# Kernel tuning notes

Measured on AMD Instinct MI355X. Metric: run time of the kernel, lower is better.

Reference implementation:

```python
import jax, jax.numpy as jnp
import numpy as np


def conv2d(x, w, b=None, stride=1, padding=0, groups=1, dilation=1):
    out = jax.lax.conv_general_dilated(
        x, w, (stride, stride), [(padding, padding), (padding, padding)],
        rhs_dilation=(dilation, dilation),
        dimension_numbers=("NCHW", "OIHW", "NCHW"),
        feature_group_count=groups)
    if b is not None:
        out = out + b[None, :, None, None]
    return out


def _l2norm(x, axis=-1, eps=1e-12):
    n = jnp.sqrt(jnp.sum(x * x, axis=axis, keepdims=True))
    return x / jnp.maximum(n, eps)


def setup_inputs() -> dict:
    B, C, H, W = 8, 384, 64, 64
    heads = 8
    C6, C2, C4 = C // 6, C // 2, C // 4
    key = jax.random.key(0)
    ks = iter(jax.random.split(key, 40))
    p = lambda shape: jax.random.normal(next(ks), shape, jnp.float32) * 0.02
    z = lambda n: jnp.zeros((n,), jnp.float32)
    inp = {
        "x": jax.random.normal(next(ks), (B, C, H, W), jnp.float32),
        "temperature": jnp.ones((heads, 1, 1), jnp.float32),
        "qkv_w": p((3 * C, C)),
        "proj_w": p((C, C)), "proj_b": z(C),
        # dwconv branch on v_: 1x1 conv then depthwise 3x3
        "dw1_w": p((C, C, 1, 1)), "dw1_b": z(C),
        "dw2_w": p((C, 1, 3, 3)), "dw2_b": z(C),
        # ChannelProjection
        "cp_in_w": p((C6, C, 1, 1)), "cp_in_b": z(C6),
        "ci1_w": p((C6, C6, 1, 1)), "ci1_b": z(C6),
        "ci2a_w": p((C6, 1, 3, 3)), "ci2a_b": z(C6),
        "ci2b_w": p((C6, 1, 7, 7)), "ci2b_b": z(C6),
        "ci2c_w": p((C6, C6, 1, 1)), "ci2c_b": z(C6),
        "cp_out_w": p((C, C6, 1, 1)), "cp_out_b": z(C),
        # SpatialProjection
        "sp_in_w": p((C2, C, 1, 1)), "sp_in_b": z(C2),
        "sp_dw_w": p((C2, 1, 3, 3)), "sp_dw_b": z(C2),
        "sp_out_w": p((C, C4, 1, 1)), "sp_out_b": z(C),
    }
    return inp


def reference(x, temperature, qkv_w, proj_w, proj_b, dw1_w, dw1_b, dw2_w, dw2_b,
              cp_in_w, cp_in_b, ci1_w, ci1_b, ci2a_w, ci2a_b, ci2b_w, ci2b_b,
              ci2c_w, ci2c_b, cp_out_w, cp_out_b, sp_in_w, sp_in_b,
              sp_dw_w, sp_dw_b, sp_out_w, sp_out_b):
    B, C, H, W = x.shape
    N = H * W
    heads = temperature.shape[0]
    hd = C // heads
    C6 = cp_in_w.shape[0]
    C2 = sp_in_w.shape[0]

    xf = x.reshape(B, C, N).transpose(0, 2, 1)            # (B,N,C)
    qkv = xf @ qkv_w.T                                     # (B,N,3C)
    qkv = qkv.reshape(B, N, 3, heads, hd).transpose(2, 0, 3, 1, 4)  # (3,B,h,N,hd)
    q = qkv[0].swapaxes(-2, -1)                            # (B,h,hd,N)
    k = qkv[1].swapaxes(-2, -1)
    v = qkv[2].swapaxes(-2, -1)
    v_ = v.reshape(B, C, H, W)

    q = _l2norm(q, axis=-1)
    k = _l2norm(k, axis=-1)
    attn = jnp.einsum("bhcn,bhdn->bhcd", q, k) * temperature  # (B,h,hd,hd)
    attn = jax.nn.softmax(attn, axis=-1)
    at = jnp.einsum("bhcd,bhdn->bhcn", attn, v)             # (B,h,hd,N)
    attened = at.transpose(0, 3, 1, 2).reshape(B, N, C)     # (B,N,C)

    conv_x = conv2d(conv2d(v_, dw1_w, dw1_b),
                    dw2_w, dw2_b, padding=1, groups=C)      # (B,C,H,W)

    # ChannelProjection on attention map
    ar = attened.swapaxes(-2, -1).reshape(B, C, H, W)
    t = conv2d(ar, cp_in_w, cp_in_b)                        # (B,C6,H,W)
    ci1 = conv2d(t.mean((2, 3), keepdims=True), ci1_w, ci1_b)  # (B,C6,1,1)
    ci2 = conv2d(t, ci2a_w, ci2a_b, padding=1, groups=C6)
    ci2 = conv2d(ci2, ci2b_w, ci2b_b, padding=9, groups=C6, dilation=3)
    ci2 = conv2d(ci2, ci2c_w, ci2c_b)
    channel_map = conv2d(t * ci1 * ci2, cp_out_w, cp_out_b)  # (B,C,H,W)

    attened = attened + channel_map.transpose(0, 2, 3, 1).reshape(B, N, C)
    cm = channel_map.mean((2, 3), keepdims=True)            # (B,C,1,1)

    # SpatialProjection on conv branch
    sp = conv2d(conv_x, sp_in_w, sp_in_b)                   # (B,C2,H,W)
    d = conv2d(sp, sp_dw_w, sp_dw_b, padding=1, groups=C2)
    x1, x2 = jnp.split(d, 2, axis=1)
    sp = conv2d(jax.nn.gelu(x1, approximate=False) * x2, sp_out_w, sp_out_b)
    spatial_map = sp.transpose(0, 2, 3, 1).reshape(B, N, C)

    attened = attened * jax.nn.sigmoid(spatial_map)
    conv_x = conv_x * jax.nn.sigmoid(cm)
    conv_x = conv_x.transpose(0, 2, 3, 1).reshape(B, N, C)

    out = (attened + conv_x) @ proj_w.T + proj_b            # (B,N,C)
    return out.transpose(0, 2, 1).reshape(B, C, H, W)
```

## Files before the change

### kernel.cpp

```cpp
#include <hip/hip_runtime.h>
#include <hip/hip_bf16.h>

typedef __bf16 bf16;
typedef __bf16 bf16x8 __attribute__((ext_vector_type(8)));
typedef float f32x4 __attribute__((ext_vector_type(4)));

#define N4 4096
#define CCH 384

struct CvtArgs {
    const float* src[9];
    bf16* dst[9];
    long gpre[10];
};

__global__ __launch_bounds__(256) void cvt_kernel(CvtArgs a, long totalGroups)
{
    long g = (long)blockIdx.x * 256 + threadIdx.x;
    if (g >= totalGroups) return;
    int lo = 0, hi = 8;
    while (lo < hi) { int mid = (lo + hi) >> 1; if (g >= a.gpre[mid + 1]) lo = mid + 1; else hi = mid; }
    long off = (g - a.gpre[lo]) << 3;
    const float* s = a.src[lo] + off;
    float4 v0 = *(const float4*)s;
    float4 v1 = *(const float4*)(s + 4);
    bf16x8 o;
    o[0] = (bf16)v0.x; o[1] = (bf16)v0.y; o[2] = (bf16)v0.z; o[3] = (bf16)v0.w;
    o[4] = (bf16)v1.x; o[5] = (bf16)v1.y; o[6] = (bf16)v1.z; o[7] = (bf16)v1.w;
    *(bf16x8*)(a.dst[lo] + off) = o;
}

__global__ __launch_bounds__(256) void gemm_bf16_kernel(
    const bf16* __restrict__ Wg, const bf16* __restrict__ Xg,
    const float* __restrict__ bias, void* __restrict__ Og,
    int K, long xStride, long oStride, int f32out)
{
    constexpr int LDP = 40;
    __shared__ bf16 Wt[64 * LDP];
    __shared__ bf16 Xt[64 * LDP];
    const int t = threadIdx.x;
    const int lin = blockIdx.x;
    const int b = lin & 7;
    const int rest = lin >> 3;
    const int nBase = (rest & 63) << 6;
    const int mBase = (rest >> 6) << 6;
    const bf16* Xb = Xg + (long)b * xStride;
    const int lane = t & 63, wv = t >> 6;
    const int wm = (wv >> 1) << 5, wn = (wv & 1) << 5;
    const int lr = lane & 15, qd = lane >> 4;
    const int wlm = t >> 2, wlk = (t & 3) << 3;
    const int xln = t & 63, xlk = (t >> 6) << 3;

    f32x4 acc[2][2] = {};

    for (int k0 = 0; k0 < K; k0 += 32) {
        bf16x8 wvv = *(const bf16x8*)(Wg + (long)(mBase + wlm) * K + k0 + wlk);
        const bf16* xp = Xb + (long)(k0 + xlk) * N4 + nBase + xln;
        bf16x8 xvv;
        #pragma unroll
        for (int j = 0; j < 8; j++) xvv[j] = xp[(long)j * N4];

        __syncthreads();
        *(bf16x8*)(&Wt[wlm * LDP + wlk]) = wvv;
        *(bf16x8*)(&Xt[xln * LDP + xlk]) = xvv;
        __syncthreads();

        bf16x8 af[2], bfr[2];
        #pragma unroll
        for (int i = 0; i < 2; i++) {
            af[i]  = *(const bf16x8*)(&Wt[(wm + i * 16 + lr) * LDP + qd * 8]);
            bfr[i] = *(const bf16x8*)(&Xt[(wn + i * 16 + lr) * LDP + qd * 8]);
        }
        #pragma unroll
        for (int i = 0; i < 2; i++)
            #pragma unroll
            for (int j = 0; j < 2; j++)
                acc[i][j] = __builtin_amdgcn_mfma_f32_16x16x32_bf16(
                    af[i], bfr[j], acc[i][j], 0, 0, 0);
    }

    #pragma unroll
    for (int i = 0; i < 2; i++)
        #pragma unroll
        for (int j = 0; j < 2; j++)
            #pragma unroll
            for (int r = 0; r < 4; r++) {
                int row = mBase + wm + i * 16 + qd * 4 + r;
                int col = nBase + wn + j * 16 + lr;
                float v = acc[i][j][r];
                if (bias) v += bias[row];
                long oi = (long)b * oStride + (long)row * N4 + col;
                if (f32out) ((float*)Og)[oi] = v;
                else        ((bf16*)Og)[oi] = (bf16)v;
            }
}

__global__ __launch_bounds__(256) void gemm128_kernel(
    const bf16* __restrict__ Wg, const bf16* __restrict__ Xg,
    const float* __restrict__ bias, void* __restrict__ Og,
    int K, long xStride, long oStride, int f32out)
{
    constexpr int LDP = 40;
    __shared__ bf16 Wt[128 * LDP];
    __shared__ bf16 Xt[128 * LDP];
    const int t = threadIdx.x;
    const int lin = blockIdx.x;
    const int b = lin & 7;
    const int rest = lin >> 3;
    const int nBase = (rest & 31) << 7;
    const int mBase = (rest >> 5) << 7;
    const bf16* Xb = Xg + (long)b * xStride;
    const int lane = t & 63, wv = t >> 6;
    const int wm = (wv >> 1) << 6, wn = (wv & 1) << 6;
    const int lr = lane & 15, qd = lane >> 4;
    const int wrow0 = t >> 2, wk = (t & 3) << 3;

    f32x4 acc[4][4] = {};

    for (int k0 = 0; k0 < K; k0 += 32) {
        bf16x8 wv0 = *(const bf16x8*)(Wg + (long)(mBase + wrow0) * K + k0 + wk);
        bf16x8 wv1 = *(const bf16x8*)(Wg + (long)(mBase + wrow0 + 64) * K + k0 + wk);
        bf16x8 xv[2];
        #pragma unroll
        for (int g = 0; g < 2; g++) {
            int slot = g * 256 + t;
            int kg = slot >> 7, nn = slot & 127;
            const bf16* xp = Xb + (long)(k0 + kg * 8) * N4 + nBase + nn;
            #pragma unroll
            for (int j = 0; j < 8; j++) xv[g][j] = xp[(long)j * N4];
        }
        __syncthreads();
        *(bf16x8*)(&Wt[wrow0 * LDP + wk]) = wv0;
        *(bf16x8*)(&Wt[(wrow0 + 64) * LDP + wk]) = wv1;
        #pragma unroll
        for (int g = 0; g < 2; g++) {
            int slot = g * 256 + t;
            int kg = slot >> 7, nn = slot & 127;
            *(bf16x8*)(&Xt[nn * LDP + kg * 8]) = xv[g];
        }
        __syncthreads();

        bf16x8 af[4], bfr[4];
        #pragma unroll
        for (int i = 0; i < 4; i++) {
            af[i]  = *(const bf16x8*)(&Wt[(wm + i * 16 + lr) * LDP + qd * 8]);
            bfr[i] = *(const bf16x8*)(&Xt[(wn + i * 16 + lr) * LDP + qd * 8]);
        }
        #pragma unroll
        for (int i = 0; i < 4; i++)
            #pragma unroll
            for (int j = 0; j < 4; j++)
                acc[i][j] = __builtin_amdgcn_mfma_f32_16x16x32_bf16(
                    af[i], bfr[j], acc[i][j], 0, 0, 0);
    }

    #pragma unroll
    for (int i = 0; i < 4; i++)
        #pragma unroll
        for (int j = 0; j < 4; j++)
            #pragma unroll
            for (int r = 0; r < 4; r++) {
                int row = mBase + wm + i * 16 + qd * 4 + r;
                int col = nBase + wn + j * 16 + lr;
                float v = acc[i][j][r];
                if (bias) v += bias[row];
                long oi = (long)b * oStride + (long)row * N4 + col;
                if (f32out) ((float*)Og)[oi] = v;
                else        ((bf16*)Og)[oi] = (bf16)v;
            }
}

__global__ __launch_bounds__(256) void rownorm_kernel(
    const bf16* __restrict__ qkv, float* __restrict__ invn)
{
    const int c = blockIdx.x, b = blockIdx.y;
    const bf16* p = qkv + (long)b * 3 * CCH * N4 + (long)c * N4;
    float s = 0.f;
    for (int i = threadIdx.x * 8; i < N4; i += 2048) {
        bf16x8 v = *(const bf16x8*)(p + i);
        #pragma unroll
        for (int e = 0; e < 8; e++) { float f = (float)v[e]; s += f * f; }
    }
    #pragma unroll
    for (int o = 32; o; o >>= 1) s += __shfl_down(s, o, 64);
    __shared__ float red[4];
    if ((threadIdx.x & 63) == 0) red[threadIdx.x >> 6] = s;
    __syncthreads();
    if (threadIdx.x == 0) {
        float tot = red[0] + red[1] + red[2] + red[3];
        invn[b * 768 + c] = 1.0f / fmaxf(sqrtf(tot), 1e-12f);
    }
}

__global__ __launch_bounds__(256) void attn_logits_kernel(
    const bf16* __restrict__ qkv, float* __restrict__ part)
{
    const int kc = blockIdx.x;
    const int bh = blockIdx.y;
    const int b = bh >> 3, h = bh & 7;
    const int t = threadIdx.x, lane = t & 63, wv = t >> 6;
    const int lr = lane & 15, qd = lane >> 4;
    const bf16* qb = qkv + (long)b * 3 * CCH * N4 + (long)h * 48 * N4;
    const bf16* kb = qb + (long)CCH * N4;
    const int k0b = (kc * 4 + wv) * 128;
    f32x4 acc[3][3] = {};
    for (int s = 0; s < 4; s++) {
        const int k0 = k0b + s * 32;
        bf16x8 a[3], bb[3];
        #pragma unroll
        for (int i = 0; i < 3; i++) {
            a[i]  = *(const bf16x8*)(qb + (long)(i * 16 + lr) * N4 + k0 + qd * 8);
            bb[i] = *(const bf16x8*)(kb + (long)(i * 16 + lr) * N4 + k0 + qd * 8);
        }
        #pragma unroll
        for (int i = 0; i < 3; i++)
            #pragma unroll
            for (int j = 0; j < 3; j++)
                acc[i][j] = __builtin_amdgcn_mfma_f32_16x16x32_bf16(
                    a[i], bb[j], acc[i][j], 0, 0, 0);
    }
    float* pp = part + ((long)bh * 32 + kc * 4 + wv) * 2304;
    #pragma unroll
    for (int i = 0; i < 3; i++)
        #pragma unroll
        for (int j = 0; j < 3; j++)
            #pragma unroll
            for (int r = 0; r < 4; r++)
                pp[(i * 16 + qd * 4 + r) * 48 + j * 16 + lr] = acc[i][j][r];
}

__global__ __launch_bounds__(256) void attn_softmax_kernel(
    const float* __restrict__ part, const float* __restrict__ invn,
    const float* __restrict__ temp, float* __restrict__ attn)
{
    __shared__ float sl[2304];
    const int bh = blockIdx.x, b = bh >> 3, h = bh & 7;
    const int t = threadIdx.x;
    const float tmp = temp[h];
    for (int idx = t; idx < 2304; idx += 256) {
        float s = 0.f;
        for (int p = 0; p < 32; p++) s += part[((long)bh * 32 + p) * 2304 + idx];
        int d = idx / 48, e = idx - d * 48;
        s *= invn[b * 768 + h * 48 + d] * invn[b * 768 + 384 + h * 48 + e] * tmp;
        sl[idx] = s;
    }
    __syncthreads();
    if (t < 48) {
        float m = -1e30f;
        #pragma unroll
        for (int e = 0; e < 48; e++) m = fmaxf(m, sl[t * 48 + e]);
        float ex[48]; float sum = 0.f;
        #pragma unroll
        for (int e = 0; e < 48; e++) { ex[e] = expf(sl[t * 48 + e] - m); sum += ex[e]; }
        float inv = 1.0f / sum;
        #pragma unroll
        for (int e = 0; e < 48; e++) attn[(long)bh * 2304 + t * 48 + e] = ex[e] * inv;
    }
}

__global__ __launch_bounds__(256) void attn_apply_kernel(
    const float* __restrict__ attn, const bf16* __restrict__ qkv,
    bf16* __restrict__ at)
{
    __shared__ float sa[2304];
    const int bh = blockIdx.y, b = bh >> 3, h = bh & 7;
    const int t = threadIdx.x;
    for (int i = t; i < 2304; i += 256) sa[i] = attn[(long)bh * 2304 + i];
    __syncthreads();
    const int n = blockIdx.x * 256 + t;
    const bf16* vb = qkv + (long)b * 3 * CCH * N4 + (long)(2 * CCH + h * 48) * N4;
    float acc[48];
    #pragma unroll
    for (int d = 0; d < 48; d++) acc[d] = 0.f;
    for (int e = 0; e < 48; e++) {
        float vv = (float)vb[(long)e * N4 + n];
        #pragma unroll
        for (int d = 0; d < 48; d++) acc[d] += sa[d * 48 + e] * vv;
    }
    bf16* ab = at + (long)b * CCH * N4 + (long)h * 48 * N4 + n;
    #pragma unroll
    for (int d = 0; d < 48; d++) ab[(long)d * N4] = (bf16)acc[d];
}

template<int S, int DIL, int PAD, int CH>
__global__ __launch_bounds__(512) void dw_conv_kernel(
    const bf16* __restrict__ in, const float* __restrict__ wt,
    const float* __restrict__ bias, bf16* __restrict__ outp)
{
    constexpr int SPAN = 8 + (S - 1) * DIL;
    constexpr int CL = (PAD + 7) / 8;
    constexpr int CR = ((S - 1) * DIL - PAD + 7) / 8;
    constexpr int NC = CL + 1 + CR;
    const int p = blockIdx.x;
    const int c = p % CH;
    const int u = threadIdx.x;
    const int y = u >> 3, x0 = (u & 7) << 3;
    const bf16* ip = in + (long)p * N4;

    float wf[S * S];
    #pragma unroll
    for (int i = 0; i < S * S; i++) wf[i] = wt[c * S * S + i];

    float acc[8];
    float bz = bias[c];
    #pragma unroll
    for (int px = 0; px < 8; px++) acc[px] = bz;

    #pragma unroll
    for (int i = 0; i < S; i++) {
        int yy = y + i * DIL - PAD;
        if (yy >= 0 && yy < 64) {
            const bf16* rp = ip + yy * 64;
            bf16 chunk[NC][8];
            #pragma unroll
            for (int cix = 0; cix < NC; cix++) {
                int xx = x0 + (cix - CL) * 8;
                if (xx >= 0 && xx < 64) {
                    *(bf16x8*)chunk[cix] = *(const bf16x8*)(rp + xx);
                } else {
                    #pragma unroll
                    for (int e = 0; e < 8; e++) chunk[cix][e] = (bf16)0.f;
                }
            }
            float w[SPAN];
            #pragma unroll
            for (int pp = 0; pp < SPAN; pp++) {
                constexpr int BASE = CL * 8 - PAD;
                int o = pp + BASE;
                w[pp] = (float)chunk[o >> 3][o & 7];
            }
            #pragma unroll
            for (int j = 0; j < S; j++) {
                float wj = wf[i * S + j];
                #pragma unroll
                for (int px = 0; px < 8; px++)
                    acc[px] += wj * w[px + j * DIL];
            }
        }
    }
    bf16x8 ov;
    #pragma unroll
    for (int px = 0; px < 8; px++) ov[px] = (bf16)acc[px];
    *(bf16x8*)(outp + (long)p * N4 + y * 64 + x0) = ov;
}

__global__ __launch_bounds__(256) void mean_kernel(
    const bf16* __restrict__ in, float* __restrict__ outp)
{
    const int Cc = gridDim.x;
    const int c = blockIdx.x, b = blockIdx.y;
    const bf16* p = in + ((long)b * Cc + c) * N4;
    float s = 0.f;
    for (int i = threadIdx.x * 8; i < N4; i += 2048) {
        bf16x8 v = *(const bf16x8*)(p + i);
        #pragma unroll
        for (int e = 0; e < 8; e++) s += (float)v[e];
    }
    #pragma unroll
    for (int o = 32; o; o >>= 1) s += __shfl_down(s, o, 64);
    __shared__ float red[4];
    if ((threadIdx.x & 63) == 0) red[threadIdx.x >> 6] = s;
    __syncthreads();
    if (threadIdx.x == 0)
        outp[b * Cc + c] = (red[0] + red[1] + red[2] + red[3]) * (1.0f / N4);
}

__global__ __launch_bounds__(64) void ci1_kernel(
    const float* __restrict__ tmean, const float* __restrict__ wt,
    const float* __restrict__ bias, float* __restrict__ ci1v)
{
    const int b = blockIdx.x, o = threadIdx.x;
    float s = bias[o];
    for (int i = 0; i < 64; i++) s += wt[o * 64 + i] * tmean[b * 64 + i];
    ci1v[b * 64 + o] = s;
}

__global__ __launch_bounds__(256) void g_eltwise_kernel(
    const bf16* __restrict__ t, const float* __restrict__ ci1v,
    const bf16* __restrict__ u3, bf16* __restrict__ g)
{
    long idx = ((long)blockIdx.x * 256 + threadIdx.x) << 3;
    float s = ci1v[idx >> 12];
    bf16x8 tv = *(const bf16x8*)(t + idx);
    bf16x8 uv = *(const bf16x8*)(u3 + idx);
    bf16x8 ov;
    #pragma unroll
    for (int e = 0; e < 8; e++) ov[e] = (bf16)((float)tv[e] * s * (float)uv[e]);
    *(bf16x8*)(g + idx) = ov;
}

__global__ __launch_bounds__(256) void gelu_mul_kernel(
    const bf16* __restrict__ dd, bf16* __restrict__ g2)
{
    long idx = ((long)blockIdx.x * 256 + threadIdx.x) << 3;
    int n = idx & 4095;
    long bc = idx >> 12;
    long b = bc / 96, cc = bc - b * 96;
    bf16x8 v1 = *(const bf16x8*)(dd + ((b * 192 + cc) << 12) + n);
    bf16x8 v2 = *(const bf16x8*)(dd + ((b * 192 + cc + 96) << 12) + n);
    bf16x8 ov;
    #pragma unroll
    for (int e = 0; e < 8; e++) {
        float x1 = (float)v1[e];
        float g = 0.5f * x1 * (1.0f + erff(x1 * 0.70710678118654752f));
        ov[e] = (bf16)(g * (float)v2[e]);
    }
    *(bf16x8*)(g2 + idx) = ov;
}

__global__ __launch_bounds__(256) void final_mix_kernel(
    bf16* __restrict__ at, const bf16* __restrict__ cmap,
    const bf16* __restrict__ smap, const bf16* __restrict__ convx,
    const float* __restrict__ cm)
{
    long idx = ((long)blockIdx.x * 256 + threadIdx.x) << 3;
    float g = 1.0f / (1.0f + expf(-cm[idx >> 12]));
    bf16x8 av = *(const bf16x8*)(at + idx);
    bf16x8 cv = *(const bf16x8*)(cmap + idx);
    bf16x8 sv = *(const bf16x8*)(smap + idx);
    bf16x8 xv = *(const bf16x8*)(convx + idx);
    bf16x8 ov;
    #pragma unroll
    for (int e = 0; e < 8; e++) {
        float a = (float)av[e] + (float)cv[e];
        float s = 1.0f / (1.0f + expf(-(float)sv[e]));
        ov[e] = (bf16)(a * s + (float)xv[e] * g);
    }
    *(bf16x8*)(at + idx) = ov;
}

extern "C" void kernel_launch(void* const* d_in, const int* in_sizes, int n_in,
                              void* d_out, int out_size, void* d_ws, size_t ws_size,
                              hipStream_t stream)
{
    const int B = 8, C = 384, N = N4, C6 = 64, C2 = 192, C4 = 96;

    char* wsp = (char*)d_ws;
    size_t off = 0;
    auto alloc = [&](size_t bytes) -> char* {
        char* p = wsp + off; off += (bytes + 255) & ~(size_t)255; return p;
    };

    const int cvtIdx[9] = {0, 2, 3, 5, 9, 17, 19, 21, 25};
    bf16* cv[9];
    CvtArgs ca;
    long gpre = 0;
    for (int i = 0; i < 9; i++) {
        int ti = cvtIdx[i];
        cv[i] = (bf16*)alloc((size_t)in_sizes[ti] * 2);
        ca.src[i] = (const float*)d_in[ti];
        ca.dst[i] = cv[i];
        ca.gpre[i] = gpre;
        gpre += in_sizes[ti] >> 3;
    }
    ca.gpre[9] = gpre;
    cvt_kernel<<<(int)((gpre + 255) / 256), 256, 0, stream>>>(ca, gpre);

    const bf16* x_bf     = cv[0];
    const bf16* qkv_w    = cv[1];
    const bf16* proj_w   = cv[2];
    const bf16* dw1_w    = cv[3];
    const bf16* cp_in_w  = cv[4];
    const bf16* ci2c_w   = cv[5];
    const bf16* cp_out_w = cv[6];
    const bf16* sp_in_w  = cv[7];
    const bf16* sp_out_w = cv[8];

    const float* temp    = (const float*)d_in[1];
    const float* proj_b  = (const float*)d_in[4];
    const float* dw1_b   = (const float*)d_in[6];
    const float* dw2_w   = (const float*)d_in[7];
    const float* dw2_b   = (const float*)d_in[8];
    const float* cp_in_b = (const float*)d_in[10];
    const float* ci1_w   = (const float*)d_in[11];
    const float* ci1_b   = (const float*)d_in[12];
    const float* ci2a_w  = (const float*)d_in[13];
    const float* ci2a_b  = (const float*)d_in[14];
    const float* ci2b_w  = (const float*)d_in[15];
    const float* ci2b_b  = (const float*)d_in[16];
    const float* ci2c_b  = (const float*)d_in[18];
    const float* cp_out_b= (const float*)d_in[20];
    const float* sp_in_b = (const float*)d_in[22];
    const float* sp_dw_w = (const float*)d_in[23];
    const float* sp_dw_b = (const float*)d_in[24];
    const float* sp_out_b= (const float*)d_in[26];

    bf16*  QKV   = (bf16*) alloc((size_t)B * 3 * C * N * 2);
    bf16*  AT    = (bf16*) alloc((size_t)B * C * N * 2);
    bf16*  CONV1 = (bf16*) alloc((size_t)B * C * N * 2);
    bf16*  CONVX = (bf16*) alloc((size_t)B * C * N * 2);
    bf16*  CMAP  = (bf16*) alloc((size_t)B * C * N * 2);
    bf16*  T     = (bf16*) alloc((size_t)B * C6 * N * 2);
    bf16*  U1    = (bf16*) alloc((size_t)B * C6 * N * 2);
    bf16*  U2    = (bf16*) alloc((size_t)B * C6 * N * 2);
    bf16*  SP    = (bf16*) alloc((size_t)B * C2 * N * 2);
    bf16*  DDb   = (bf16*) alloc((size_t)B * C2 * N * 2);
    float* PART  = (float*)alloc((size_t)64 * 32 * 2304 * 4);
    float* ATTN  = (float*)alloc((size_t)64 * 2304 * 4);
    float* INVN  = (float*)alloc((size_t)B * 768 * 4);
    float* TMEAN = (float*)alloc((size_t)B * 64 * 4);
    float* CI1V  = (float*)alloc((size_t)B * 64 * 4);
    float* CMv   = (float*)alloc((size_t)B * C * 4);
    bf16* SMAP = CONV1;
    bf16* G2   = SP;
    bf16* U3   = U1;
    bf16* G    = U2;

    gemm128_kernel<<<8 * 32 * 9, 256, 0, stream>>>(
        qkv_w, x_bf, nullptr, QKV, 384, (long)C * N, (long)3 * C * N, 0);
    rownorm_kernel<<<dim3(768, 8), 256, 0, stream>>>(QKV, INVN);
    attn_logits_kernel<<<dim3(8, 64), 256, 0, stream>>>(QKV, PART);
    attn_softmax_kernel<<<64, 256, 0, stream>>>(PART, INVN, temp, ATTN);
    attn_apply_kernel<<<dim3(16, 64), 256, 0, stream>>>(ATTN, QKV, AT);
    gemm128_kernel<<<8 * 32 * 3, 256, 0, stream>>>(
        dw1_w, QKV + (size_t)2 * C * N, dw1_b, CONV1, 384, (long)3 * C * N, (long)C * N, 0);
    dw_conv_kernel<3, 1, 1, 384><<<B * 384, 512, 0, stream>>>(CONV1, dw2_w, dw2_b, CONVX);
    gemm_bf16_kernel<<<8 * 64 * 1, 256, 0, stream>>>(
        cp_in_w, AT, cp_in_b, T, 384, (long)C * N, (long)C6 * N, 0);
    mean_kernel<<<dim3(64, 8), 256, 0, stream>>>(T, TMEAN);
    ci1_kernel<<<8, 64, 0, stream>>>(TMEAN, ci1_w, ci1_b, CI1V);
    dw_conv_kernel<3, 1, 1, 64><<<B * 64, 512, 0, stream>>>(T, ci2a_w, ci2a_b, U1);
    dw_conv_kernel<7, 3, 9, 64><<<B * 64, 512, 0, stream>>>(U1, ci2b_w, ci2b_b, U2);
    gemm_bf16_kernel<<<8 * 64 * 1, 256, 0, stream>>>(
        ci2c_w, U2, ci2c_b, U3, 64, (long)C6 * N, (long)C6 * N, 0);
    g_eltwise_kernel<<<1024, 256, 0, stream>>>(T, CI1V, U3, G);
    gemm128_kernel<<<8 * 32 * 3, 256, 0, stream>>>(
        cp_out_w, G, cp_out_b, CMAP, 64, (long)C6 * N, (long)C * N, 0);
    mean_kernel<<<dim3(384, 8), 256, 0, stream>>>(CMAP, CMv);
    gemm_bf16_kernel<<<8 * 64 * 3, 256, 0, stream>>>(
        sp_in_w, CONVX, sp_in_b, SP, 384, (long)C * N, (long)C2 * N, 0);
    dw_conv_kernel<3, 1, 1, 192><<<B * 192, 512, 0, stream>>>(SP, sp_dw_w, sp_dw_b, DDb);
    gelu_mul_kernel<<<1536, 256, 0, stream>>>(DDb, G2);
    gemm128_kernel<<<8 * 32 * 3, 256, 0, stream>>>(
        sp_out_w, G2, sp_out_b, SMAP, 96, (long)C4 * N, (long)C * N, 0);
    final_mix_kernel<<<6144, 256, 0, stream>>>(AT, CMAP, SMAP, CONVX, CMv);
    gemm128_kernel<<<8 * 32 * 3, 256, 0, stream>>>(
        proj_w, AT, proj_b, d_out, 384, (long)C * N, (long)C * N, 1);
}
```

Measured before the change: 516.6 us.

## Switch intermediates to channels-last layout with direct-load NT GEMMs

```diff
diff --git a/kernel.cpp b/kernel.cpp
--- a/kernel.cpp
+++ b/kernel.cpp
@@ -2,23 +2,23 @@
 #include <hip/hip_bf16.h>
 
 typedef __bf16 bf16;
+typedef __bf16 bf16x4 __attribute__((ext_vector_type(4)));
 typedef __bf16 bf16x8 __attribute__((ext_vector_type(8)));
 typedef float f32x4 __attribute__((ext_vector_type(4)));
 
-#define N4 4096
-#define CCH 384
+#define NPIX 4096
 
 struct CvtArgs {
-    const float* src[9];
-    bf16* dst[9];
-    long gpre[10];
+    const float* src[8];
+    bf16* dst[8];
+    long gpre[9];
 };
 
 __global__ __launch_bounds__(256) void cvt_kernel(CvtArgs a, long totalGroups)
 {
     long g = (long)blockIdx.x * 256 + threadIdx.x;
     if (g >= totalGroups) return;
-    int lo = 0, hi = 8;
+    int lo = 0, hi = 7;
     while (lo < hi) { int mid = (lo + hi) >> 1; if (g >= a.gpre[mid + 1]) lo = mid + 1; else hi = mid; }
     long off = (g - a.gpre[lo]) << 3;
     const float* s = a.src[lo] + off;
@@ -30,196 +30,218 @@
     *(bf16x8*)(a.dst[lo] + off) = o;
 }
 
-__global__ __launch_bounds__(256) void gemm_bf16_kernel(
-    const bf16* __restrict__ Wg, const bf16* __restrict__ Xg,
-    const float* __restrict__ bias, void* __restrict__ Og,
-    int K, long xStride, long oStride, int f32out)
-{
-    constexpr int LDP = 40;
-    __shared__ bf16 Wt[64 * LDP];
-    __shared__ bf16 Xt[64 * LDP];
+__global__ __launch_bounds__(256) void xpose_in_kernel(
+    const float* __restrict__ x, bf16* __restrict__ XT)
+{
+    __shared__ bf16 Lt[64][72];
+    const int n0 = blockIdx.x << 6, c0 = blockIdx.y << 6, b = blockIdx.z;
+    const int t = threadIdx.x;
+    const int rr = t >> 4, q4 = (t & 15) << 2;
+    #pragma unroll
+    for (int it = 0; it < 4; it++) {
+        int ci = rr + it * 16;
+        float4 v = *(const float4*)(x + ((long)(b * 384 + c0 + ci) << 12) + n0 + q4);
+        Lt[ci][q4 + 0] = (bf16)v.x; Lt[ci][q4 + 1] = (bf16)v.y;
+        Lt[ci][q4 + 2] = (bf16)v.z; Lt[ci][q4 + 3] = (bf16)v.w;
+    }
+    __syncthreads();
+    #pragma unroll
+    for (int it = 0; it < 4; it++) {
+        int ni = rr + it * 16;
+        bf16x4 o;
+        #pragma unroll
+        for (int e = 0; e < 4; e++) o[e] = Lt[q4 + e][ni];
+        *(bf16x4*)(XT + ((long)(b * NPIX + n0 + ni)) * 384 + c0 + q4) = o;
+    }
+}
+
+__global__ __launch_bounds__(256) void xpose_out_kernel(
+    const bf16* __restrict__ PRJ, float* __restrict__ outp)
+{
+    __shared__ bf16 Lt[64][72];
+    const int n0 = blockIdx.x << 6, c0 = blockIdx.y << 6, b = blockIdx.z;
+    const int t = threadIdx.x;
+    const int rr = t >> 4, q4 = (t & 15) << 2;
+    #pragma unroll
+    for (int it = 0; it < 4; it++) {
+        int ni = rr + it * 16;
+        bf16x4 v = *(const bf16x4*)(PRJ + ((long)(b * NPIX + n0 + ni)) * 384 + c0 + q4);
+        #pragma unroll
+        for (int e = 0; e < 4; e++) Lt[ni][q4 + e] = v[e];
+    }
+    __syncthreads();
+    #pragma unroll
+    for (int it = 0; it < 4; it++) {
+        int ci = rr + it * 16;
+        float4 f;
+        f.x = (float)Lt[q4 + 0][ci]; f.y = (float)Lt[q4 + 1][ci];
+        f.z = (float)Lt[q4 + 2][ci]; f.w = (float)Lt[q4 + 3][ci];
+        *(float4*)(outp + ((long)(b * 384 + c0 + ci) << 12) + n0 + q4) = f;
+    }
+}
+
+__global__ __launch_bounds__(256) void gemm_nt128_kernel(
+    const bf16* __restrict__ Xg, long xBatch, int xRow,
+    const bf16* __restrict__ Wg, int K,
+    const float* __restrict__ bias, bf16* __restrict__ Og,
+    long oBatch, int oRow, int nTiles)
+{
     const int t = threadIdx.x;
     const int lin = blockIdx.x;
     const int b = lin & 7;
     const int rest = lin >> 3;
-    const int nBase = (rest & 63) << 6;
-    const int mBase = (rest >> 6) << 6;
-    const bf16* Xb = Xg + (long)b * xStride;
+    const int nBase = (rest % nTiles) << 7;
+    const int mBase = (rest / nTiles) << 7;
     const int lane = t & 63, wv = t >> 6;
-    const int wm = (wv >> 1) << 5, wn = (wv & 1) << 5;
+    const int nOff = (wv & 1) << 6, mOff = (wv >> 1) << 6;
     const int lr = lane & 15, qd = lane >> 4;
-    const int wlm = t >> 2, wlk = (t & 3) << 3;
-    const int xln = t & 63, xlk = (t >> 6) << 3;
-
-    f32x4 acc[2][2] = {};
-
+    const bf16* Ab = Xg + (long)b * xBatch;
+
+    f32x4 acc[4][4] = {};
     for (int k0 = 0; k0 < K; k0 += 32) {
-        bf16x8 wvv = *(const bf16x8*)(Wg + (long)(mBase + wlm) * K + k0 + wlk);
-        const bf16* xp = Xb + (long)(k0 + xlk) * N4 + nBase + xln;
-        bf16x8 xvv;
-        #pragma unroll
-        for (int j = 0; j < 8; j++) xvv[j] = xp[(long)j * N4];
-
-        __syncthreads();
-        *(bf16x8*)(&Wt[wlm * LDP + wlk]) = wvv;
-        *(bf16x8*)(&Xt[xln * LDP + xlk]) = xvv;
-        __syncthreads();
-
-        bf16x8 af[2], bfr[2];
-        #pragma unroll
-        for (int i = 0; i < 2; i++) {
-            af[i]  = *(const bf16x8*)(&Wt[(wm + i * 16 + lr) * LDP + qd * 8]);
-            bfr[i] = *(const bf16x8*)(&Xt[(wn + i * 16 + lr) * LDP + qd * 8]);
-        }
-        #pragma unroll
-        for (int i = 0; i < 2; i++)
-            #pragma unroll
-            for (int j = 0; j < 2; j++)
-                acc[i][j] = __builtin_amdgcn_mfma_f32_16x16x32_bf16(
-                    af[i], bfr[j], acc[i][j], 0, 0, 0);
-    }
-
-    #pragma unroll
-    for (int i = 0; i < 2; i++)
-        #pragma unroll
-        for (int j = 0; j < 2; j++)
-            #pragma unroll
-            for (int r = 0; r < 4; r++) {
-                int row = mBase + wm + i * 16 + qd * 4 + r;
-                int col = nBase + wn + j * 16 + lr;
-                float v = acc[i][j][r];
-                if (bias) v += bias[row];
-                long oi = (long)b * oStride + (long)row * N4 + col;
-                if (f32out) ((float*)Og)[oi] = v;
-                else        ((bf16*)Og)[oi] = (bf16)v;
-            }
-}
-
-__global__ __launch_bounds__(256) void gemm128_kernel(
-    const bf16* __restrict__ Wg, const bf16* __restrict__ Xg,
-    const float* __restrict__ bias, void* __restrict__ Og,
-    int K, long xStride, long oStride, int f32out)
-{
-    constexpr int LDP = 40;
-    __shared__ bf16 Wt[128 * LDP];
-    __shared__ bf16 Xt[128 * LDP];
+        bf16x8 a[4], bb[4];
+        #pragma unroll
+        for (int i = 0; i < 4; i++)
+            a[i] = *(const bf16x8*)(Ab + (long)(nBase + nOff + i * 16 + lr) * xRow + k0 + qd * 8);
+        #pragma unroll
+        for (int j = 0; j < 4; j++)
+            bb[j] = *(const bf16x8*)(Wg + (long)(mBase + mOff + j * 16 + lr) * K + k0 + qd * 8);
+        #pragma unroll
+        for (int i = 0; i < 4; i++)
+            #pragma unroll
+            for (int j = 0; j < 4; j++)
+                acc[i][j] = __builtin_amdgcn_mfma_f32_16x16x32_bf16(a[i], bb[j], acc[i][j], 0, 0, 0);
+    }
+
+    float bj[4];
+    #pragma unroll
+    for (int j = 0; j < 4; j++) bj[j] = bias ? bias[mBase + mOff + j * 16 + lr] : 0.f;
+
+    bf16* Ob = Og + (long)b * oBatch;
+    #pragma unroll
+    for (int i = 0; i < 4; i++)
+        #pragma unroll
+        for (int r = 0; r < 4; r++) {
+            long rowOff = (long)(nBase + nOff + i * 16 + qd * 4 + r) * oRow;
+            #pragma unroll
+            for (int j = 0; j < 4; j++)
+                Ob[rowOff + mBase + mOff + j * 16 + lr] = (bf16)(acc[i][j][r] + bj[j]);
+        }
+}
+
+__global__ __launch_bounds__(256) void gemm_nt64_kernel(
+    const bf16* __restrict__ Xg, long xBatch, int xRow,
+    const bf16* __restrict__ Wg, int K,
+    const float* __restrict__ bias, bf16* __restrict__ Og,
+    long oBatch, int oRow, int nTiles)
+{
     const int t = threadIdx.x;
     const int lin = blockIdx.x;
     const int b = lin & 7;
     const int rest = lin >> 3;
-    const int nBase = (rest & 31) << 7;
-    const int mBase = (rest >> 5) << 7;
-    const bf16* Xb = Xg + (long)b * xStride;
+    const int nBase = (rest % nTiles) << 7;
+    const int mBase = (rest / nTiles) << 6;
     const int lane = t & 63, wv = t >> 6;
-    const int wm = (wv >> 1) << 6, wn = (wv & 1) << 6;
+    const int nOff = wv << 5;
     const int lr = lane & 15, qd = lane >> 4;
-    const int wrow0 = t >> 2, wk = (t & 3) << 3;
-
-    f32x4 acc[4][4] = {};
-
+    const bf16* Ab = Xg + (long)b * xBatch;
+
+    f32x4 acc[2][4] = {};
     for (int k0 = 0; k0 < K; k0 += 32) {
-        bf16x8 wv0 = *(const bf16x8*)(Wg + (long)(mBase + wrow0) * K + k0 + wk);
-        bf16x8 wv1 = *(const bf16x8*)(Wg + (long)(mBase + wrow0 + 64) * K + k0 + wk);
-        bf16x8 xv[2];
-        #pragma unroll
-        for (int g = 0; g < 2; g++) {
-            int slot = g * 256 + t;
-            int kg = slot >> 7, nn = slot & 127;
-            const bf16* xp = Xb + (long)(k0 + kg * 8) * N4 + nBase + nn;
-            #pragma unroll
-            for (int j = 0; j < 8; j++) xv[g][j] = xp[(long)j * N4];
-        }
-        __syncthreads();
-        *(bf16x8*)(&Wt[wrow0 * LDP + wk]) = wv0;
-        *(bf16x8*)(&Wt[(wrow0 + 64) * LDP + wk]) = wv1;
-        #pragma unroll
-        for (int g = 0; g < 2; g++) {
-            int slot = g * 256 + t;
-            int kg = slot >> 7, nn = slot & 127;
-            *(bf16x8*)(&Xt[nn * LDP + kg * 8]) = xv[g];
-        }
-        __syncthreads();
-
-        bf16x8 af[4], bfr[4];
-        #pragma unroll
-        for (int i = 0; i < 4; i++) {
-            af[i]  = *(const bf16x8*)(&Wt[(wm + i * 16 + lr) * LDP + qd * 8]);
-            bfr[i] = *(const bf16x8*)(&Xt[(wn + i * 16 + lr) * LDP + qd * 8]);
-        }
-        #pragma unroll
-        for (int i = 0; i < 4; i++)
+        bf16x8 a[2], bb[4];
+        #pragma unroll
+        for (int i = 0; i < 2; i++)
+            a[i] = *(const bf16x8*)(Ab + (long)(nBase + nOff + i * 16 + lr) * xRow + k0 + qd * 8);
+        #pragma unroll
+        for (int j = 0; j < 4; j++)
+            bb[j] = *(const bf16x8*)(Wg + (long)(mBase + j * 16 + lr) * K + k0 + qd * 8);
+        #pragma unroll
+        for (int i = 0; i < 2; i++)
             #pragma unroll
             for (int j = 0; j < 4; j++)
-                acc[i][j] = __builtin_amdgcn_mfma_f32_16x16x32_bf16(
-                    af[i], bfr[j], acc[i][j], 0, 0, 0);
-    }
-
-    #pragma unroll
-    for (int i = 0; i < 4; i++)
-        #pragma unroll
-        for (int j = 0; j < 4; j++)
-            #pragma unroll
-            for (int r = 0; r < 4; r++) {
-                int row = mBase + wm + i * 16 + qd * 4 + r;
-                int col = nBase + wn + j * 16 + lr;
-                float v = acc[i][j][r];
-                if (bias) v += bias[row];
-                long oi = (long)b * oStride + (long)row * N4 + col;
-                if (f32out) ((float*)Og)[oi] = v;
-                else        ((bf16*)Og)[oi] = (bf16)v;
-            }
+                acc[i][j] = __builtin_amdgcn_mfma_f32_16x16x32_bf16(a[i], bb[j], acc[i][j], 0, 0, 0);
+    }
+
+    float bj[4];
+    #pragma unroll
+    for (int j = 0; j < 4; j++) bj[j] = bias ? bias[mBase + j * 16 + lr] : 0.f;
+
+    bf16* Ob = Og + (long)b * oBatch;
+    #pragma unroll
+    for (int i = 0; i < 2; i++)
+        #pragma unroll
+        for (int r = 0; r < 4; r++) {
+            long rowOff = (long)(nBase + nOff + i * 16 + qd * 4 + r) * oRow;
+            #pragma unroll
+            for (int j = 0; j < 4; j++)
+                Ob[rowOff + mBase + j * 16 + lr] = (bf16)(acc[i][j][r] + bj[j]);
+        }
 }
 
 __global__ __launch_bounds__(256) void rownorm_kernel(
-    const bf16* __restrict__ qkv, float* __restrict__ invn)
-{
-    const int c = blockIdx.x, b = blockIdx.y;
-    const bf16* p = qkv + (long)b * 3 * CCH * N4 + (long)c * N4;
+    const bf16* __restrict__ qkvt, float* __restrict__ invn)
+{
+    const int b = blockIdx.y;
+    const int c = (blockIdx.x << 6) + (threadIdx.x & 63);
+    const int g = threadIdx.x >> 6;
     float s = 0.f;
-    for (int i = threadIdx.x * 8; i < N4; i += 2048) {
-        bf16x8 v = *(const bf16x8*)(p + i);
-        #pragma unroll
-        for (int e = 0; e < 8; e++) { float f = (float)v[e]; s += f * f; }
-    }
-    #pragma unroll
-    for (int o = 32; o; o >>= 1) s += __shfl_down(s, o, 64);
-    __shared__ float red[4];
-    if ((threadIdx.x & 63) == 0) red[threadIdx.x >> 6] = s;
-    __syncthreads();
-    if (threadIdx.x == 0) {
-        float tot = red[0] + red[1] + red[2] + red[3];
-        invn[b * 768 + c] = 1.0f / fmaxf(sqrtf(tot), 1e-12f);
+    const bf16* base = qkvt + (long)b * NPIX * 1152 + c;
+    for (int n = g; n < NPIX; n += 4) {
+        float v = (float)base[(long)n * 1152];
+        s += v * v;
+    }
+    __shared__ float red[256];
+    red[threadIdx.x] = s;
+    __syncthreads();
+    if (threadIdx.x < 64) {
+        float tot = red[threadIdx.x] + red[threadIdx.x + 64] + red[threadIdx.x + 128] + red[threadIdx.x + 192];
+        invn[b * 768 + (blockIdx.x << 6) + threadIdx.x] = 1.0f / fmaxf(sqrtf(tot), 1e-12f);
     }
 }
 
 __global__ __launch_bounds__(256) void attn_logits_kernel(
-    const bf16* __restrict__ qkv, float* __restrict__ part)
-{
+    const bf16* __restrict__ qkvt, float* __restrict__ part)
+{
+    __shared__ bf16 QK[96 * 264];
     const int kc = blockIdx.x;
     const int bh = blockIdx.y;
     const int b = bh >> 3, h = bh & 7;
     const int t = threadIdx.x, lane = t & 63, wv = t >> 6;
     const int lr = lane & 15, qd = lane >> 4;
-    const bf16* qb = qkv + (long)b * 3 * CCH * N4 + (long)h * 48 * N4;
-    const bf16* kb = qb + (long)CCH * N4;
-    const int k0b = (kc * 4 + wv) * 128;
+    const long qbase = (long)b * NPIX * 1152 + h * 48;
+
     f32x4 acc[3][3] = {};
-    for (int s = 0; s < 4; s++) {
-        const int k0 = k0b + s * 32;
-        bf16x8 a[3], bb[3];
-        #pragma unroll
-        for (int i = 0; i < 3; i++) {
-            a[i]  = *(const bf16x8*)(qb + (long)(i * 16 + lr) * N4 + k0 + qd * 8);
-            bb[i] = *(const bf16x8*)(kb + (long)(i * 16 + lr) * N4 + k0 + qd * 8);
-        }
-        #pragma unroll
-        for (int i = 0; i < 3; i++)
-            #pragma unroll
-            for (int j = 0; j < 3; j++)
-                acc[i][j] = __builtin_amdgcn_mfma_f32_16x16x32_bf16(
-                    a[i], bb[j], acc[i][j], 0, 0, 0);
-    }
-    float* pp = part + ((long)bh * 32 + kc * 4 + wv) * 2304;
+    for (int it = 0; it < 4; it++) {
+        const int nBase = kc * 1024 + it * 256;
+        __syncthreads();
+        for (int cc = 0; cc < 12; cc++) {
+            int chunk = cc * 256 + t;
+            int which = chunk >= 1536;
+            int r2 = chunk - which * 1536;
+            int n_l = r2 / 6, cgi = r2 - n_l * 6;
+            bf16x8 v = *(const bf16x8*)(qkvt + qbase + (long)(nBase + n_l) * 1152 + which * 384 + cgi * 8);
+            bf16* dst = &QK[(which * 48 + cgi * 8) * 264 + n_l];
+            #pragma unroll
+            for (int e = 0; e < 8; e++) dst[e * 264] = v[e];
+        }
+        __syncthreads();
+        const int n0 = wv << 6;
+        #pragma unroll
+        for (int ks = 0; ks < 2; ks++) {
+            bf16x8 a[3], bb[3];
+            #pragma unroll
+            for (int i = 0; i < 3; i++) {
+                a[i]  = *(const bf16x8*)(&QK[(i * 16 + lr) * 264 + n0 + ks * 32 + qd * 8]);
+                bb[i] = *(const bf16x8*)(&QK[(48 + i * 16 + lr) * 264 + n0 + ks * 32 + qd * 8]);
+            }
+            #pragma unroll
+            for (int i = 0; i < 3; i++)
+                #pragma unroll
+                for (int j = 0; j < 3; j++)
+                    acc[i][j] = __builtin_amdgcn_mfma_f32_16x16x32_bf16(a[i], bb[j], acc[i][j], 0, 0, 0);
+        }
+    }
+    float* pp = part + ((long)bh * 16 + kc * 4 + wv) * 2304;
     #pragma unroll
     for (int i = 0; i < 3; i++)
         #pragma unroll
@@ -239,7 +261,8 @@
     const float tmp = temp[h];
     for (int idx = t; idx < 2304; idx += 256) {
         float s = 0.f;
-        for (int p = 0; p < 32; p++) s += part[((long)bh * 32 + p) * 2304 + idx];
+        #pragma unroll
+        for (int p = 0; p < 16; p++) s += part[((long)bh * 16 + p) * 2304 + idx];
         int d = idx / 48, e = idx - d * 48;
         s *= invn[b * 768 + h * 48 + d] * invn[b * 768 + 384 + h * 48 + e] * tmp;
         sl[idx] = s;
@@ -259,7 +282,7 @@
 }
 
 __global__ __launch_bounds__(256) void attn_apply_kernel(
-    const float* __restrict__ attn, const bf16* __restrict__ qkv,
+    const float* __restrict__ attn, const bf16* __restrict__ qkvt,
     bf16* __restrict__ at)
 {
     __shared__ float sa[2304];
@@ -268,101 +291,123 @@
     for (int i = t; i < 2304; i += 256) sa[i] = attn[(long)bh * 2304 + i];
     __syncthreads();
     const int n = blockIdx.x * 256 + t;
-    const bf16* vb = qkv + (long)b * 3 * CCH * N4 + (long)(2 * CCH + h * 48) * N4;
-    float acc[48];
-    #pragma unroll
-    for (int d = 0; d < 48; d++) acc[d] = 0.f;
-    for (int e = 0; e < 48; e++) {
-        float vv = (float)vb[(long)e * N4 + n];
-        #pragma unroll
-        for (int d = 0; d < 48; d++) acc[d] += sa[d * 48 + e] * vv;
-    }
-    bf16* ab = at + (long)b * CCH * N4 + (long)h * 48 * N4 + n;
-    #pragma unroll
-    for (int d = 0; d < 48; d++) ab[(long)d * N4] = (bf16)acc[d];
-}
-
-template<int S, int DIL, int PAD, int CH>
-__global__ __launch_bounds__(512) void dw_conv_kernel(
+    const bf16* vp = qkvt + ((long)(b * NPIX + n)) * 1152 + 768 + h * 48;
+    float vv[48];
+    #pragma unroll
+    for (int cg = 0; cg < 6; cg++) {
+        bf16x8 v = *(const bf16x8*)(vp + cg * 8);
+        #pragma unroll
+        for (int e = 0; e < 8; e++) vv[cg * 8 + e] = (float)v[e];
+    }
+    bf16* ap = at + ((long)(b * NPIX + n)) * 384 + h * 48;
+    #pragma unroll
+    for (int cg = 0; cg < 6; cg++) {
+        bf16x8 o;
+        #pragma unroll
+        for (int dd = 0; dd < 8; dd++) {
+            int d = cg * 8 + dd;
+            float acc = 0.f;
+            for (int e = 0; e < 48; e++) acc += sa[d * 48 + e] * vv[e];
+            o[dd] = (bf16)acc;
+        }
+        *(bf16x8*)(ap + cg * 8) = o;
+    }
+}
+
+template<int CH>
+__global__ __launch_bounds__(256) void dw3_kernel(
     const bf16* __restrict__ in, const float* __restrict__ wt,
     const float* __restrict__ bias, bf16* __restrict__ outp)
 {
-    constexpr int SPAN = 8 + (S - 1) * DIL;
-    constexpr int CL = (PAD + 7) / 8;
-    constexpr int CR = ((S - 1) * DIL - PAD + 7) / 8;
-    constexpr int NC = CL + 1 + CR;
-    const int p = blockIdx.x;
-    const int c = p % CH;
-    const int u = threadIdx.x;
-    const int y = u >> 3, x0 = (u & 7) << 3;
-    const bf16* ip = in + (long)p * N4;
-
-    float wf[S * S];
-    #pragma unroll
-    for (int i = 0; i < S * S; i++) wf[i] = wt[c * S * S + i];
+    constexpr int G = CH / 8;
+    const int gid = blockIdx.x * 256 + threadIdx.x;
+    const int p = gid / G, cg = gid - p * G;
+    const int b = p >> 12, pix = p & 4095, y = pix >> 6, xx = pix & 63;
+
+    float wr[9][8];
+    #pragma unroll
+    for (int e = 0; e < 8; e++)
+        #pragma unroll
+        for (int tp = 0; tp < 9; tp++)
+            wr[tp][e] = wt[(cg * 8 + e) * 9 + tp];
 
     float acc[8];
-    float bz = bias[c];
-    #pragma unroll
-    for (int px = 0; px < 8; px++) acc[px] = bz;
-
-    #pragma unroll
-    for (int i = 0; i < S; i++) {
-        int yy = y + i * DIL - PAD;
-        if (yy >= 0 && yy < 64) {
-            const bf16* rp = ip + yy * 64;
-            bf16 chunk[NC][8];
-            #pragma unroll
-            for (int cix = 0; cix < NC; cix++) {
-                int xx = x0 + (cix - CL) * 8;
-                if (xx >= 0 && xx < 64) {
-                    *(bf16x8*)chunk[cix] = *(const bf16x8*)(rp + xx);
-                } else {
-                    #pragma unroll
-                    for (int e = 0; e < 8; e++) chunk[cix][e] = (bf16)0.f;
-                }
-            }
-            float w[SPAN];
-            #pragma unroll
-            for (int pp = 0; pp < SPAN; pp++) {
-                constexpr int BASE = CL * 8 - PAD;
-                int o = pp + BASE;
-                w[pp] = (float)chunk[o >> 3][o & 7];
-            }
-            #pragma unroll
-            for (int j = 0; j < S; j++) {
-                float wj = wf[i * S + j];
-                #pragma unroll
-                for (int px = 0; px < 8; px++)
-                    acc[px] += wj * w[px + j * DIL];
-            }
-        }
-    }
-    bf16x8 ov;
-    #pragma unroll
-    for (int px = 0; px < 8; px++) ov[px] = (bf16)acc[px];
-    *(bf16x8*)(outp + (long)p * N4 + y * 64 + x0) = ov;
+    #pragma unroll
+    for (int e = 0; e < 8; e++) acc[e] = bias[cg * 8 + e];
+
+    const bf16* ib = in + ((long)b << 12) * CH;
+    #pragma unroll
+    for (int dy = -1; dy <= 1; dy++) {
+        int yy = y + dy;
+        if (yy < 0 || yy >= 64) continue;
+        #pragma unroll
+        for (int dx = -1; dx <= 1; dx++) {
+            int x2 = xx + dx;
+            if (x2 < 0 || x2 >= 64) continue;
+            bf16x8 v = *(const bf16x8*)(ib + (long)(yy * 64 + x2) * CH + cg * 8);
+            int tp = (dy + 1) * 3 + (dx + 1);
+            #pragma unroll
+            for (int e = 0; e < 8; e++) acc[e] += wr[tp][e] * (float)v[e];
+        }
+    }
+    bf16x8 o;
+    #pragma unroll
+    for (int e = 0; e < 8; e++) o[e] = (bf16)acc[e];
+    *(bf16x8*)(outp + (long)p * CH + cg * 8) = o;
+}
+
+__global__ __launch_bounds__(256) void dw7_kernel(
+    const bf16* __restrict__ in, const float* __restrict__ wt,
+    const float* __restrict__ bias, bf16* __restrict__ outp)
+{
+    __shared__ float wf[64 * 49];
+    __shared__ float bf[64];
+    for (int i = threadIdx.x; i < 64 * 49; i += 256) wf[i] = wt[i];
+    if (threadIdx.x < 64) bf[threadIdx.x] = bias[threadIdx.x];
+    __syncthreads();
+
+    const int gid = blockIdx.x * 256 + threadIdx.x;
+    const int cg = gid & 7, p = gid >> 3;
+    const int b = p >> 12, pix = p & 4095, y = pix >> 6, xx = pix & 63;
+
+    float acc[8];
+    #pragma unroll
+    for (int e = 0; e < 8; e++) acc[e] = bf[cg * 8 + e];
+
+    const bf16* ib = in + ((long)b << 12) * 64;
+    for (int i = 0; i < 7; i++) {
+        int yy = y + i * 3 - 9;
+        if (yy < 0 || yy >= 64) continue;
+        for (int j = 0; j < 7; j++) {
+            int x2 = xx + j * 3 - 9;
+            if (x2 < 0 || x2 >= 64) continue;
+            bf16x8 v = *(const bf16x8*)(ib + (long)(yy * 64 + x2) * 64 + cg * 8);
+            int tp = i * 7 + j;
+            #pragma unroll
+            for (int e = 0; e < 8; e++) acc[e] += wf[(cg * 8 + e) * 49 + tp] * (float)v[e];
+        }
+    }
+    bf16x8 o;
+    #pragma unroll
+    for (int e = 0; e < 8; e++) o[e] = (bf16)acc[e];
+    *(bf16x8*)(outp + (long)p * 64 + cg * 8) = o;
 }
 
 __global__ __launch_bounds__(256) void mean_kernel(
-    const bf16* __restrict__ in, float* __restrict__ outp)
-{
-    const int Cc = gridDim.x;
-    const int c = blockIdx.x, b = blockIdx.y;
-    const bf16* p = in + ((long)b * Cc + c) * N4;
+    const bf16* __restrict__ in, float* __restrict__ outp, int CH)
+{
+    const int b = blockIdx.y;
+    const int c = (blockIdx.x << 6) + (threadIdx.x & 63);
+    const int g = threadIdx.x >> 6;
     float s = 0.f;
-    for (int i = threadIdx.x * 8; i < N4; i += 2048) {
-        bf16x8 v = *(const bf16x8*)(p + i);
-        #pragma unroll
-        for (int e = 0; e < 8; e++) s += (float)v[e];
-    }
-    #pragma unroll
-    for (int o = 32; o; o >>= 1) s += __shfl_down(s, o, 64);
-    __shared__ float red[4];
-    if ((threadIdx.x & 63) == 0) red[threadIdx.x >> 6] = s;
-    __syncthreads();
-    if (threadIdx.x == 0)
-        outp[b * Cc + c] = (red[0] + red[1] + red[2] + red[3]) * (1.0f / N4);
+    const bf16* base = in + (long)b * NPIX * CH + c;
+    for (int n = g; n < NPIX; n += 4) s += (float)base[(long)n * CH];
+    __shared__ float red[256];
+    red[threadIdx.x] = s;
+    __syncthreads();
+    if (threadIdx.x < 64)
+        outp[b * CH + (blockIdx.x << 6) + threadIdx.x] =
+            (red[threadIdx.x] + red[threadIdx.x + 64] + red[threadIdx.x + 128] + red[threadIdx.x + 192]) * (1.0f / NPIX);
 }
 
 __global__ __launch_bounds__(64) void ci1_kernel(
@@ -379,25 +424,27 @@
     const bf16* __restrict__ t, const float* __restrict__ ci1v,
     const bf16* __restrict__ u3, bf16* __restrict__ g)
 {
-    long idx = ((long)blockIdx.x * 256 + threadIdx.x) << 3;
-    float s = ci1v[idx >> 12];
+    unsigned idx = ((unsigned)blockIdx.x * 256 + threadIdx.x) << 3;
+    unsigned row = idx >> 6, c0 = idx & 63;
+    const float* cp = ci1v + (row >> 12) * 64 + c0;
+    float4 s0 = *(const float4*)cp;
+    float4 s1 = *(const float4*)(cp + 4);
+    float sv[8] = {s0.x, s0.y, s0.z, s0.w, s1.x, s1.y, s1.z, s1.w};
     bf16x8 tv = *(const bf16x8*)(t + idx);
     bf16x8 uv = *(const bf16x8*)(u3 + idx);
     bf16x8 ov;
     #pragma unroll
-    for (int e = 0; e < 8; e++) ov[e] = (bf16)((float)tv[e] * s * (float)uv[e]);
+    for (int e = 0; e < 8; e++) ov[e] = (bf16)((float)tv[e] * sv[e] * (float)uv[e]);
     *(bf16x8*)(g + idx) = ov;
 }
 
 __global__ __launch_bounds__(256) void gelu_mul_kernel(
     const bf16* __restrict__ dd, bf16* __restrict__ g2)
 {
-    long idx = ((long)blockIdx.x * 256 + threadIdx.x) << 3;
-    int n = idx & 4095;
-    long bc = idx >> 12;
-    long b = bc / 96, cc = bc - b * 96;
-    bf16x8 v1 = *(const bf16x8*)(dd + ((b * 192 + cc) << 12) + n);
-    bf16x8 v2 = *(const bf16x8*)(dd + ((b * 192 + cc + 96) << 12) + n);
+    unsigned idx = ((unsigned)blockIdx.x * 256 + threadIdx.x) << 3;
+    unsigned row = idx / 96, off = idx - row * 96;
+    bf16x8 v1 = *(const bf16x8*)(dd + (long)row * 192 + off);
+    bf16x8 v2 = *(const bf16x8*)(dd + (long)row * 192 + off + 96);
     bf16x8 ov;
     #pragma unroll
     for (int e = 0; e < 8; e++) {
@@ -413,8 +460,12 @@
     const bf16* __restrict__ smap, const bf16* __restrict__ convx,
     const float* __restrict__ cm)
 {
-    long idx = ((long)blockIdx.x * 256 + threadIdx.x) << 3;
-    float g = 1.0f / (1.0f + expf(-cm[idx >> 12]));
+    unsigned idx = ((unsigned)blockIdx.x * 256 + threadIdx.x) << 3;
+    unsigned row = idx / 384, c0 = idx - row * 384;
+    const float* cp = cm + (row >> 12) * 384 + c0;
+    float4 s0 = *(const float4*)cp;
+    float4 s1 = *(const float4*)(cp + 4);
+    float gv[8] = {s0.x, s0.y, s0.z, s0.w, s1.x, s1.y, s1.z, s1.w};
     bf16x8 av = *(const bf16x8*)(at + idx);
     bf16x8 cv = *(const bf16x8*)(cmap + idx);
     bf16x8 sv = *(const bf16x8*)(smap + idx);
@@ -424,6 +475,7 @@
     for (int e = 0; e < 8; e++) {
         float a = (float)av[e] + (float)cv[e];
         float s = 1.0f / (1.0f + expf(-(float)sv[e]));
+        float g = 1.0f / (1.0f + expf(-gv[e]));
         ov[e] = (bf16)(a * s + (float)xv[e] * g);
     }
     *(bf16x8*)(at + idx) = ov;
@@ -433,7 +485,8 @@
                               void* d_out, int out_size, void* d_ws, size_t ws_size,
                               hipStream_t stream)
 {
-    const int B = 8, C = 384, N = N4, C6 = 64, C2 = 192, C4 = 96;
+    const int B = 8;
+    const long NB = (long)B * NPIX;
 
     char* wsp = (char*)d_ws;
     size_t off = 0;
@@ -441,31 +494,24 @@
         char* p = wsp + off; off += (bytes + 255) & ~(size_t)255; return p;
     };
 
-    const int cvtIdx[9] = {0, 2, 3, 5, 9, 17, 19, 21, 25};
-    bf16* cv[9];
+    const int cvtIdx[8] = {2, 3, 5, 9, 17, 19, 21, 25};
+    bf16* wcv[8];
     CvtArgs ca;
     long gpre = 0;
-    for (int i = 0; i < 9; i++) {
+    for (int i = 0; i < 8; i++) {
         int ti = cvtIdx[i];
-        cv[i] = (bf16*)alloc((size_t)in_sizes[ti] * 2);
+        wcv[i] = (bf16*)alloc((size_t)in_sizes[ti] * 2);
         ca.src[i] = (const float*)d_in[ti];
-        ca.dst[i] = cv[i];
+        ca.dst[i] = wcv[i];
         ca.gpre[i] = gpre;
         gpre += in_sizes[ti] >> 3;
     }
-    ca.gpre[9] = gpre;
-    cvt_kernel<<<(int)((gpre + 255) / 256), 256, 0, stream>>>(ca, gpre);
-
-    const bf16* x_bf     = cv[0];
-    const bf16* qkv_w    = cv[1];
-    const bf16* proj_w   = cv[2];
-    const bf16* dw1_w    = cv[3];
-    const bf16* cp_in_w  = cv[4];
-    const bf16* ci2c_w   = cv[5];
-    const bf16* cp_out_w = cv[6];
-    const bf16* sp_in_w  = cv[7];
-    const bf16* sp_out_w = cv[8];
-
+    ca.gpre[8] = gpre;
+
+    const bf16 *qkv_w = wcv[0], *proj_w = wcv[1], *dw1_w = wcv[2], *cp_in_w = wcv[3],
+               *ci2c_w = wcv[4], *cp_out_w = wcv[5], *sp_in_w = wcv[6], *sp_out_w = wcv[7];
+
+    const float* xf      = (const float*)d_in[0];
     const float* temp    = (const float*)d_in[1];
     const float* proj_b  = (const float*)d_in[4];
     const float* dw1_b   = (const float*)d_in[6];
@@ -485,55 +531,61 @@
     const float* sp_dw_b = (const float*)d_in[24];
     const float* sp_out_b= (const float*)d_in[26];
 
-    bf16*  QKV   = (bf16*) alloc((size_t)B * 3 * C * N * 2);
-    bf16*  AT    = (bf16*) alloc((size_t)B * C * N * 2);
-    bf16*  CONV1 = (bf16*) alloc((size_t)B * C * N * 2);
-    bf16*  CONVX = (bf16*) alloc((size_t)B * C * N * 2);
-    bf16*  CMAP  = (bf16*) alloc((size_t)B * C * N * 2);
-    bf16*  T     = (bf16*) alloc((size_t)B * C6 * N * 2);
-    bf16*  U1    = (bf16*) alloc((size_t)B * C6 * N * 2);
-    bf16*  U2    = (bf16*) alloc((size_t)B * C6 * N * 2);
-    bf16*  SP    = (bf16*) alloc((size_t)B * C2 * N * 2);
-    bf16*  DDb   = (bf16*) alloc((size_t)B * C2 * N * 2);
-    float* PART  = (float*)alloc((size_t)64 * 32 * 2304 * 4);
+    bf16*  XT    = (bf16*) alloc(NB * 384 * 2);
+    bf16*  QKVT  = (bf16*) alloc(NB * 1152 * 2 + 256);
+    bf16*  AT    = (bf16*) alloc(NB * 384 * 2);
+    bf16*  CONV1 = (bf16*) alloc(NB * 384 * 2);
+    bf16*  CONVX = (bf16*) alloc(NB * 384 * 2);
+    bf16*  CMAP  = (bf16*) alloc(NB * 384 * 2);
+    bf16*  T     = (bf16*) alloc(NB * 64 * 2);
+    bf16*  U1    = (bf16*) alloc(NB * 64 * 2);
+    bf16*  U2    = (bf16*) alloc(NB * 64 * 2);
+    bf16*  SP    = (bf16*) alloc(NB * 192 * 2);
+    bf16*  DDb   = (bf16*) alloc(NB * 192 * 2);
+    float* PART  = (float*)alloc((size_t)64 * 16 * 2304 * 4);
     float* ATTN  = (float*)alloc((size_t)64 * 2304 * 4);
     float* INVN  = (float*)alloc((size_t)B * 768 * 4);
     float* TMEAN = (float*)alloc((size_t)B * 64 * 4);
     float* CI1V  = (float*)alloc((size_t)B * 64 * 4);
-    float* CMv   = (float*)alloc((size_t)B * C * 4);
+    float* CMv   = (float*)alloc((size_t)B * 384 * 4);
     bf16* SMAP = CONV1;
     bf16* G2   = SP;
     bf16* U3   = U1;
     bf16* G    = U2;
-
-    gemm128_kernel<<<8 * 32 * 9, 256, 0, stream>>>(
-        qkv_w, x_bf, nullptr, QKV, 384, (long)C * N, (long)3 * C * N, 0);
-    rownorm_kernel<<<dim3(768, 8), 256, 0, stream>>>(QKV, INVN);
-    attn_logits_kernel<<<dim3(8, 64), 256, 0, stream>>>(QKV, PART);
+    bf16* PRJ  = QKVT;
+
+    cvt_kernel<<<(int)((gpre + 255) / 256), 256, 0, stream>>>(ca, gpre);
+    xpose_in_kernel<<<dim3(64, 6, 8), 256, 0, stream>>>(xf, XT);
+
+    gemm_nt128_kernel<<<8 * 32 * 9, 256, 0, stream>>>(
+        XT, NB / B * 384, 384, qkv_w, 384, nullptr, QKVT, (long)NPIX * 1152, 1152, 32);
+    rownorm_kernel<<<dim3(12, 8), 256, 0, stream>>>(QKVT, INVN);
+    attn_logits_kernel<<<dim3(4, 64), 256, 0, stream>>>(QKVT, PART);
     attn_softmax_kernel<<<64, 256, 0, stream>>>(PART, INVN, temp, ATTN);
-    attn_apply_kernel<<<dim3(16, 64), 256, 0, stream>>>(ATTN, QKV, AT);
-    gemm128_kernel<<<8 * 32 * 3, 256, 0, stream>>>(
-        dw1_w, QKV + (size_t)2 * C * N, dw1_b, CONV1, 384, (long)3 * C * N, (long)C * N, 0);
-    dw_conv_kernel<3, 1, 1, 384><<<B * 384, 512, 0, stream>>>(CONV1, dw2_w, dw2_b, CONVX);
-    gemm_bf16_kernel<<<8 * 64 * 1, 256, 0, stream>>>(
-        cp_in_w, AT, cp_in_b, T, 384, (long)C * N, (long)C6 * N, 0);
-    mean_kernel<<<dim3(64, 8), 256, 0, stream>>>(T, TMEAN);
+    attn_apply_kernel<<<dim3(16, 64), 256, 0, stream>>>(ATTN, QKVT, AT);
+    gemm_nt128_kernel<<<8 * 32 * 3, 256, 0, stream>>>(
+        QKVT + 768, (long)NPIX * 1152, 1152, dw1_w, 384, dw1_b, CONV1, (long)NPIX * 384, 384, 32);
+    dw3_kernel<384><<<6144, 256, 0, stream>>>(CONV1, dw2_w, dw2_b, CONVX);
+    gemm_nt64_kernel<<<8 * 32, 256, 0, stream>>>(
+        AT, (long)NPIX * 384, 384, cp_in_w, 384, cp_in_b, T, (long)NPIX * 64, 64, 32);
+    mean_kernel<<<dim3(1, 8), 256, 0, stream>>>(T, TMEAN, 64);
     ci1_kernel<<<8, 64, 0, stream>>>(TMEAN, ci1_w, ci1_b, CI1V);
-    dw_conv_kernel<3, 1, 1, 64><<<B * 64, 512, 0, stream>>>(T, ci2a_w, ci2a_b, U1);
-    dw_conv_kernel<7, 3, 9, 64><<<B * 64, 512, 0, stream>>>(U1, ci2b_w, ci2b_b, U2);
-    gemm_bf16_kernel<<<8 * 64 * 1, 256, 0, stream>>>(
-        ci2c_w, U2, ci2c_b, U3, 64, (long)C6 * N, (long)C6 * N, 0);
+    dw3_kernel<64><<<1024, 256, 0, stream>>>(T, ci2a_w, ci2a_b, U1);
+    dw7_kernel<<<1024, 256, 0, stream>>>(U1, ci2b_w, ci2b_b, U2);
+    gemm_nt64_kernel<<<8 * 32, 256, 0, stream>>>(
+        U2, (long)NPIX * 64, 64, ci2c_w, 64, ci2c_b, U3, (long)NPIX * 64, 64, 32);
     g_eltwise_kernel<<<1024, 256, 0, stream>>>(T, CI1V, U3, G);
-    gemm128_kernel<<<8 * 32 * 3, 256, 0, stream>>>(
-        cp_out_w, G, cp_out_b, CMAP, 64, (long)C6 * N, (long)C * N, 0);
-    mean_kernel<<<dim3(384, 8), 256, 0, stream>>>(CMAP, CMv);
-    gemm_bf16_kernel<<<8 * 64 * 3, 256, 0, stream>>>(
-        sp_in_w, CONVX, sp_in_b, SP, 384, (long)C * N, (long)C2 * N, 0);
-    dw_conv_kernel<3, 1, 1, 192><<<B * 192, 512, 0, stream>>>(SP, sp_dw_w, sp_dw_b, DDb);
+    gemm_nt128_kernel<<<8 * 32 * 3, 256, 0, stream>>>(
+        G, (long)NPIX * 64, 64, cp_out_w, 64, cp_out_b, CMAP, (long)NPIX * 384, 384, 32);
+    mean_kernel<<<dim3(6, 8), 256, 0, stream>>>(CMAP, CMv, 384);
+    gemm_nt64_kernel<<<8 * 32 * 3, 256, 0, stream>>>(
+        CONVX, (long)NPIX * 384, 384, sp_in_w, 384, sp_in_b, SP, (long)NPIX * 192, 192, 32);
+    dw3_kernel<192><<<3072, 256, 0, stream>>>(SP, sp_dw_w, sp_dw_b, DDb);
     gelu_mul_kernel<<<1536, 256, 0, stream>>>(DDb, G2);
-    gemm128_kernel<<<8 * 32 * 3, 256, 0, stream>>>(
-        sp_out_w, G2, sp_out_b, SMAP, 96, (long)C4 * N, (long)C * N, 0);
+    gemm_nt128_kernel<<<8 * 32 * 3, 256, 0, stream>>>(
+        G2, (long)NPIX * 96, 96, sp_out_w, 96, sp_out_b, SMAP, (long)NPIX * 384, 384, 32);
     final_mix_kernel<<<6144, 256, 0, stream>>>(AT, CMAP, SMAP, CONVX, CMv);
-    gemm128_kernel<<<8 * 32 * 3, 256, 0, stream>>>(
-        proj_w, AT, proj_b, d_out, 384, (long)C * N, (long)C * N, 1);
-}
+    gemm_nt128_kernel<<<8 * 32 * 3, 256, 0, stream>>>(
+        AT, (long)NPIX * 384, 384, proj_w, 384, proj_b, PRJ, (long)NPIX * 384, 384, 32);
+    xpose_out_kernel<<<dim3(64, 6, 8), 256, 0, stream>>>(PRJ, (float*)d_out);
+}
```

Measured after the change: 1.402 ms. 171% more time.
